# Performance work log

Measured on AMD Instinct MI355X. Metric: run time of the kernel, lower is better.

Reference implementation:

```python
import jax, jax.numpy as jnp
import numpy as np

TOP_K = 4

def setup_inputs() -> dict:
    key = jax.random.key(0)
    k1, k2, k3, k4 = jax.random.split(key, 4)
    B, S, D, E, H, O = 4, 2048, 1024, 8, 512, 1024
    x = jax.random.normal(k1, (B, S, D), dtype=jnp.float32)
    wg = jax.random.normal(k2, (E, D), dtype=jnp.float32) * 0.02
    w1 = jax.random.normal(k3, (E, H, D), dtype=jnp.float32) * 0.02
    w2 = jax.random.normal(k4, (E, O, H), dtype=jnp.float32) * 0.02
    return {"x": x, "wg": wg, "w1": w1, "w2": w2}

def reference(x, wg, w1, w2):
    # x: [B, S, D]; wg: [E, D]; w1: [E, H, D]; w2: [E, O, H]
    B, S, D = x.shape
    E = wg.shape[0]
    xt = x.reshape(B * S, D)                       # [N, D]
    logits = xt @ wg.T                              # [N, E] gate logits
    _, idx = jax.lax.top_k(logits, TOP_K)           # [N, k] selected experts
    N = xt.shape[0]
    # membership mask: 1.0 where expert e is among the token's top-k
    mask = jnp.zeros((N, E), dtype=x.dtype).at[jnp.arange(N)[:, None], idx].set(1.0)
    # dense per-expert FFN (relu MLP), then combine with unweighted sum over
    # the k selected experts (the original sums top-k outputs without gate weights)
    h = jax.nn.relu(jnp.einsum('nd,ehd->neh', xt, w1))   # [N, E, H]
    y = jnp.einsum('neh,eoh->neo', h, w2)                # [N, E, O]
    out = jnp.einsum('neo,ne->no', y, mask)              # [N, O]
    return out.reshape(B, S, -1)
```

## Files before the change

kernel.cpp:

```cpp
#include <hip/hip_runtime.h>

typedef float f32x4 __attribute__((ext_vector_type(4)));
typedef short bf16x8 __attribute__((ext_vector_type(8)));

#define NTOK 8192
#define DIM  1024
#define NE   8
#define NH   512
#define NO   1024

static __device__ __forceinline__ unsigned short f2bf(float f) {
  unsigned u = __float_as_uint(f);
  u += 0x7fffu + ((u >> 16) & 1u);
  return (unsigned short)(u >> 16);
}
static __device__ __forceinline__ unsigned pk2(float a, float b) {
  return (unsigned)f2bf(a) | ((unsigned)f2bf(b) << 16);
}

static __device__ __forceinline__ f32x4 mfma_bf16(bf16x8 a, bf16x8 b, f32x4 c) {
  return __builtin_amdgcn_mfma_f32_16x16x32_bf16(a, b, c, 0, 0, 0);
}

__global__ __launch_bounds__(256) void gate_kernel(
    const float* __restrict__ x, const float* __restrict__ wg,
    float* __restrict__ mask)
{
  const int lane = threadIdx.x & 63;
  const int wv = threadIdx.x >> 6;
  const int n = blockIdx.x * 4 + wv;
  const float* xr = x + (size_t)n * DIM;
  float4 v[4];
#pragma unroll
  for (int i = 0; i < 4; ++i) v[i] = *(const float4*)(xr + i * 256 + lane * 4);
  double logit[NE];
#pragma unroll
  for (int e = 0; e < NE; ++e) {
    const float* wr = wg + e * DIM;
    double s = 0.0;
#pragma unroll
    for (int i = 0; i < 4; ++i) {
      float4 g = *(const float4*)(wr + i * 256 + lane * 4);
      s += (double)v[i].x * g.x + (double)v[i].y * g.y +
           (double)v[i].z * g.z + (double)v[i].w * g.w;
    }
#pragma unroll
    for (int off = 32; off; off >>= 1) s += __shfl_down(s, off);
    logit[e] = s;
  }
  if (lane == 0) {
    unsigned sel = 0;
#pragma unroll
    for (int t = 0; t < 4; ++t) {
      int best = 0; double bv = -1.0e300;
#pragma unroll
      for (int e = 0; e < NE; ++e)
        if (!((sel >> e) & 1) && logit[e] > bv) { bv = logit[e]; best = e; }
      sel |= 1u << best;
    }
#pragma unroll
    for (int e = 0; e < NE; ++e)
      mask[(size_t)n * NE + e] = ((sel >> e) & 1) ? 1.0f : 0.0f;
  }
}

__global__ __launch_bounds__(256) void pack_w1_kernel(
    const float* __restrict__ w1, unsigned short* __restrict__ w1p)
{
  int t = blockIdx.x * 256 + threadIdx.x;
  int lane = t & 63, ks = (t >> 6) & 31, nt = (t >> 11) & 31, e = t >> 16;
  int r = nt * 16 + (lane & 15);
  int c = ks * 32 + (lane >> 4) * 8;
  const float* src = w1 + ((size_t)(e * 512 + r)) * 1024 + c;
  float4 f0 = *(const float4*)src;
  float4 f1 = *(const float4*)(src + 4);
  uint4 v;
  v.x = pk2(f0.x, f0.y); v.y = pk2(f0.z, f0.w);
  v.z = pk2(f1.x, f1.y); v.w = pk2(f1.z, f1.w);
  *(uint4*)(w1p + (size_t)t * 8) = v;
}

__global__ __launch_bounds__(256) void pack_w2_kernel(
    const float* __restrict__ w2, unsigned short* __restrict__ w2p)
{
  int t = blockIdx.x * 256 + threadIdx.x;
  int lane = t & 63, ks = (t >> 6) & 15, ot = (t >> 10) & 63, e = t >> 16;
  int o = ot * 16 + (lane & 15);
  int h = ks * 32 + (lane >> 4) * 8;
  const float* src = w2 + ((size_t)(e * 1024 + o)) * 512 + h;
  float4 f0 = *(const float4*)src;
  float4 f1 = *(const float4*)(src + 4);
  uint4 v;
  v.x = pk2(f0.x, f0.y); v.y = pk2(f0.z, f0.w);
  v.z = pk2(f1.x, f1.y); v.w = pk2(f1.z, f1.w);
  *(uint4*)(w2p + (size_t)t * 8) = v;
}

__global__ __launch_bounds__(1024, 4) void moe_ffn(
    const float* __restrict__ x, const unsigned short* __restrict__ w1p,
    const unsigned short* __restrict__ w2p, const float* __restrict__ mask,
    float* __restrict__ out)
{
  __shared__ unsigned short xs[64 * 64 * 8];
  __shared__ unsigned short hs[32 * 64 * 8];
  __shared__ float mk[32 * NE];

  const int tid = threadIdx.x;
  const int lane = tid & 63;
  const int wv = tid >> 6;
  const int row0 = blockIdx.x * 32;
  const int arow = lane & 15;
  const int kch = lane >> 4;

#pragma unroll
  for (int i = 0; i < 4; ++i) {
    int c = i * 1024 + tid;
    int r = c >> 7;
    int ch = c & 127;
    const float* src = x + (size_t)(row0 + r) * DIM + ch * 8;
    float4 f0 = *(const float4*)src;
    float4 f1 = *(const float4*)(src + 4);
    uint4 v;
    v.x = pk2(f0.x, f0.y); v.y = pk2(f0.z, f0.w);
    v.z = pk2(f1.x, f1.y); v.w = pk2(f1.z, f1.w);
    int f = (ch >> 2) * 2 + (r >> 4);
    int l = ((ch & 3) << 4) | (r & 15);
    *(uint4*)(xs + ((size_t)(f * 64 + l)) * 8) = v;
  }
  if (tid < 32 * NE) mk[tid] = mask[(size_t)row0 * NE + tid];
  __syncthreads();

  f32x4 oacc[2][4];
#pragma unroll
  for (int m = 0; m < 2; ++m)
#pragma unroll
    for (int n = 0; n < 4; ++n) oacc[m][n] = f32x4{0.f, 0.f, 0.f, 0.f};

  for (int e = 0; e < NE; ++e) {
    f32x4 hacc[2][2];
#pragma unroll
    for (int m = 0; m < 2; ++m)
#pragma unroll
      for (int n = 0; n < 2; ++n) hacc[m][n] = f32x4{0.f, 0.f, 0.f, 0.f};

    const unsigned short* b1 = w1p + ((size_t)(e * 32 + wv * 2) * 32) * 64 * 8;
#pragma unroll 4
    for (int ks = 0; ks < 32; ++ks) {
      bf16x8 a0 = *(const bf16x8*)(xs + ((size_t)((ks * 2 + 0) * 64 + lane)) * 8);
      bf16x8 a1 = *(const bf16x8*)(xs + ((size_t)((ks * 2 + 1) * 64 + lane)) * 8);
      bf16x8 b0 = *(const bf16x8*)(b1 + ((size_t)(0 * 32 + ks) * 64 + lane) * 8);
      bf16x8 b2 = *(const bf16x8*)(b1 + ((size_t)(1 * 32 + ks) * 64 + lane) * 8);
      hacc[0][0] = mfma_bf16(a0, b0, hacc[0][0]);
      hacc[1][0] = mfma_bf16(a1, b0, hacc[1][0]);
      hacc[0][1] = mfma_bf16(a0, b2, hacc[0][1]);
      hacc[1][1] = mfma_bf16(a1, b2, hacc[1][1]);
    }
    __syncthreads();

#pragma unroll
    for (int m = 0; m < 2; ++m)
#pragma unroll
      for (int n = 0; n < 2; ++n)
#pragma unroll
        for (int j = 0; j < 4; ++j) {
          float v = fmaxf(hacc[m][n][j], 0.0f) * mk[(m * 16 + kch * 4 + j) * NE + e];
          int l2 = ((n * 2 + (arow >> 3)) << 4) | (kch * 4 + j);
          hs[((size_t)((wv * 2 + m) * 64 + l2)) * 8 + (arow & 7)] = f2bf(v);
        }
    __syncthreads();

    const unsigned short* b2p = w2p + ((size_t)(e * 64 + wv * 4) * 16) * 64 * 8;
#pragma unroll 4
    for (int ks = 0; ks < 16; ++ks) {
      bf16x8 a0 = *(const bf16x8*)(hs + ((size_t)((ks * 2 + 0) * 64 + lane)) * 8);
      bf16x8 a1 = *(const bf16x8*)(hs + ((size_t)((ks * 2 + 1) * 64 + lane)) * 8);
#pragma unroll
      for (int n = 0; n < 4; ++n) {
        bf16x8 b = *(const bf16x8*)(b2p + ((size_t)(n * 16 + ks) * 64 + lane) * 8);
        oacc[0][n] = mfma_bf16(a0, b, oacc[0][n]);
        oacc[1][n] = mfma_bf16(a1, b, oacc[1][n]);
      }
    }
  }

#pragma unroll
  for (int m = 0; m < 2; ++m)
#pragma unroll
    for (int n = 0; n < 4; ++n)
#pragma unroll
      for (int j = 0; j < 4; ++j) {
        int row = row0 + m * 16 + kch * 4 + j;
        int col = wv * 64 + n * 16 + arow;
        out[(size_t)row * NO + col] = oacc[m][n][j];
      }
}

extern "C" void kernel_launch(void* const* d_in, const int* in_sizes, int n_in,
                              void* d_out, int out_size, void* d_ws, size_t ws_size,
                              hipStream_t stream) {
  (void)in_sizes; (void)n_in; (void)out_size; (void)ws_size;
  const float* x  = (const float*)d_in[0];
  const float* wg = (const float*)d_in[1];
  const float* w1 = (const float*)d_in[2];
  const float* w2 = (const float*)d_in[3];
  float* out = (float*)d_out;
  char* ws = (char*)d_ws;
  unsigned short* w1p = (unsigned short*)ws;
  unsigned short* w2p = (unsigned short*)(ws + ((size_t)8 << 20));
  float* mask = (float*)(ws + ((size_t)16 << 20));

  gate_kernel<<<2048, 256, 0, stream>>>(x, wg, mask);
  pack_w1_kernel<<<2048, 256, 0, stream>>>(w1, w1p);
  pack_w2_kernel<<<2048, 256, 0, stream>>>(w2, w2p);
  moe_ffn<<<256, 1024, 0, stream>>>(x, w1p, w2p, mask, out);
}
```

Before: 200.5 us.

## Retile MoE FFN to 64-row blocks split over output halves with bitmask gating

The FFN kernel now processes 64 tokens per block, with each block computing half of the output columns. Waves are arranged as a 4x4 grid over rows and columns, and the hidden dimension is processed in two halves per expert. The aim is more weight reuse per global load and more MFMAs per A fragment. The gate now writes a one-byte expert bitmask per token instead of eight floats, which cuts mask traffic and shared memory. In exchange, the first GEMM (x·W1) is recomputed by both column-half blocks, which doubles that work, and LDS use rises for the larger x tile.

```diff
diff --git a/kernel.cpp b/kernel.cpp
--- a/kernel.cpp
+++ b/kernel.cpp
@@ -24,7 +24,7 @@
 
 __global__ __launch_bounds__(256) void gate_kernel(
     const float* __restrict__ x, const float* __restrict__ wg,
-    float* __restrict__ mask)
+    unsigned char* __restrict__ msk8)
 {
   const int lane = threadIdx.x & 63;
   const int wv = threadIdx.x >> 6;
@@ -58,9 +58,7 @@
         if (!((sel >> e) & 1) && logit[e] > bv) { bv = logit[e]; best = e; }
       sel |= 1u << best;
     }
-#pragma unroll
-    for (int e = 0; e < NE; ++e)
-      mask[(size_t)n * NE + e] = ((sel >> e) & 1) ? 1.0f : 0.0f;
+    msk8[n] = (unsigned char)sel;
   }
 }
 
@@ -98,22 +96,24 @@
 
 __global__ __launch_bounds__(1024, 4) void moe_ffn(
     const float* __restrict__ x, const unsigned short* __restrict__ w1p,
-    const unsigned short* __restrict__ w2p, const float* __restrict__ mask,
+    const unsigned short* __restrict__ w2p, const unsigned char* __restrict__ msk8,
     float* __restrict__ out)
 {
-  __shared__ unsigned short xs[64 * 64 * 8];
+  __shared__ unsigned short xs[128 * 64 * 8];
   __shared__ unsigned short hs[32 * 64 * 8];
-  __shared__ float mk[32 * NE];
 
   const int tid = threadIdx.x;
   const int lane = tid & 63;
   const int wv = tid >> 6;
-  const int row0 = blockIdx.x * 32;
+  const int rw4 = wv & 3;
+  const int cw4 = wv >> 2;
+  const int row0 = (blockIdx.x >> 1) * 64;
+  const int z = blockIdx.x & 1;
   const int arow = lane & 15;
   const int kch = lane >> 4;
 
 #pragma unroll
-  for (int i = 0; i < 4; ++i) {
+  for (int i = 0; i < 8; ++i) {
     int c = i * 1024 + tid;
     int r = c >> 7;
     int ch = c & 127;
@@ -123,76 +123,74 @@
     uint4 v;
     v.x = pk2(f0.x, f0.y); v.y = pk2(f0.z, f0.w);
     v.z = pk2(f1.x, f1.y); v.w = pk2(f1.z, f1.w);
-    int f = (ch >> 2) * 2 + (r >> 4);
+    int f = (ch >> 2) * 4 + (r >> 4);
     int l = ((ch & 3) << 4) | (r & 15);
     *(uint4*)(xs + ((size_t)(f * 64 + l)) * 8) = v;
   }
-  if (tid < 32 * NE) mk[tid] = mask[(size_t)row0 * NE + tid];
+  const unsigned mbits = *(const unsigned*)(msk8 + row0 + rw4 * 16 + kch * 4);
   __syncthreads();
 
-  f32x4 oacc[2][4];
-#pragma unroll
-  for (int m = 0; m < 2; ++m)
-#pragma unroll
-    for (int n = 0; n < 4; ++n) oacc[m][n] = f32x4{0.f, 0.f, 0.f, 0.f};
+  const unsigned short* xp = xs + lane * 8;
+  const unsigned short* hp = hs + lane * 8;
+
+  f32x4 oacc[8];
+#pragma unroll
+  for (int n = 0; n < 8; ++n) oacc[n] = f32x4{0.f, 0.f, 0.f, 0.f};
 
   for (int e = 0; e < NE; ++e) {
-    f32x4 hacc[2][2];
-#pragma unroll
-    for (int m = 0; m < 2; ++m)
-#pragma unroll
-      for (int n = 0; n < 2; ++n) hacc[m][n] = f32x4{0.f, 0.f, 0.f, 0.f};
-
-    const unsigned short* b1 = w1p + ((size_t)(e * 32 + wv * 2) * 32) * 64 * 8;
-#pragma unroll 4
-    for (int ks = 0; ks < 32; ++ks) {
-      bf16x8 a0 = *(const bf16x8*)(xs + ((size_t)((ks * 2 + 0) * 64 + lane)) * 8);
-      bf16x8 a1 = *(const bf16x8*)(xs + ((size_t)((ks * 2 + 1) * 64 + lane)) * 8);
-      bf16x8 b0 = *(const bf16x8*)(b1 + ((size_t)(0 * 32 + ks) * 64 + lane) * 8);
-      bf16x8 b2 = *(const bf16x8*)(b1 + ((size_t)(1 * 32 + ks) * 64 + lane) * 8);
-      hacc[0][0] = mfma_bf16(a0, b0, hacc[0][0]);
-      hacc[1][0] = mfma_bf16(a1, b0, hacc[1][0]);
-      hacc[0][1] = mfma_bf16(a0, b2, hacc[0][1]);
-      hacc[1][1] = mfma_bf16(a1, b2, hacc[1][1]);
-    }
-    __syncthreads();
-
-#pragma unroll
-    for (int m = 0; m < 2; ++m)
-#pragma unroll
-      for (int n = 0; n < 2; ++n)
+#pragma unroll
+    for (int hh = 0; hh < 2; ++hh) {
+      f32x4 hacc[4];
+#pragma unroll
+      for (int n = 0; n < 4; ++n) hacc[n] = f32x4{0.f, 0.f, 0.f, 0.f};
+
+      const unsigned short* pb =
+          w1p + ((size_t)(e * 32 + hh * 16 + cw4 * 4) * 32) * 512 + lane * 8;
+#pragma unroll 2
+      for (int ks = 0; ks < 32; ++ks) {
+        bf16x8 a = *(const bf16x8*)(xp + (ks * 4 + rw4) * 512);
+#pragma unroll
+        for (int n = 0; n < 4; ++n) {
+          bf16x8 b = *(const bf16x8*)(pb + (size_t)n * 16384 + ks * 512);
+          hacc[n] = mfma_bf16(a, b, hacc[n]);
+        }
+      }
+      __syncthreads();
+
+#pragma unroll
+      for (int n = 0; n < 4; ++n)
 #pragma unroll
         for (int j = 0; j < 4; ++j) {
-          float v = fmaxf(hacc[m][n][j], 0.0f) * mk[(m * 16 + kch * 4 + j) * NE + e];
-          int l2 = ((n * 2 + (arow >> 3)) << 4) | (kch * 4 + j);
-          hs[((size_t)((wv * 2 + m) * 64 + l2)) * 8 + (arow & 7)] = f2bf(v);
+          float v = fmaxf(hacc[n][j], 0.0f);
+          v = ((mbits >> (j * 8 + e)) & 1u) ? v : 0.0f;
+          int f = (cw4 * 2 + (n >> 1)) * 4 + rw4;
+          int l2 = (((n & 1) * 2 + (arow >> 3)) << 4) | (kch * 4 + j);
+          hs[((size_t)(f * 64 + l2)) * 8 + (arow & 7)] = f2bf(v);
         }
-    __syncthreads();
-
-    const unsigned short* b2p = w2p + ((size_t)(e * 64 + wv * 4) * 16) * 64 * 8;
-#pragma unroll 4
-    for (int ks = 0; ks < 16; ++ks) {
-      bf16x8 a0 = *(const bf16x8*)(hs + ((size_t)((ks * 2 + 0) * 64 + lane)) * 8);
-      bf16x8 a1 = *(const bf16x8*)(hs + ((size_t)((ks * 2 + 1) * 64 + lane)) * 8);
-#pragma unroll
-      for (int n = 0; n < 4; ++n) {
-        bf16x8 b = *(const bf16x8*)(b2p + ((size_t)(n * 16 + ks) * 64 + lane) * 8);
-        oacc[0][n] = mfma_bf16(a0, b, oacc[0][n]);
-        oacc[1][n] = mfma_bf16(a1, b, oacc[1][n]);
+      __syncthreads();
+
+      const unsigned short* pc =
+          w2p + ((size_t)((e * 64 + z * 32 + cw4 * 8) * 16 + hh * 8)) * 512 + lane * 8;
+#pragma unroll 2
+      for (int ks2 = 0; ks2 < 8; ++ks2) {
+        bf16x8 a = *(const bf16x8*)(hp + (ks2 * 4 + rw4) * 512);
+#pragma unroll
+        for (int n = 0; n < 8; ++n) {
+          bf16x8 b = *(const bf16x8*)(pc + (size_t)n * 8192 + ks2 * 512);
+          oacc[n] = mfma_bf16(a, b, oacc[n]);
+        }
       }
     }
   }
 
 #pragma unroll
-  for (int m = 0; m < 2; ++m)
-#pragma unroll
-    for (int n = 0; n < 4; ++n)
-#pragma unroll
-      for (int j = 0; j < 4; ++j) {
-        int row = row0 + m * 16 + kch * 4 + j;
-        int col = wv * 64 + n * 16 + arow;
-        out[(size_t)row * NO + col] = oacc[m][n][j];
-      }
+  for (int n = 0; n < 8; ++n)
+#pragma unroll
+    for (int j = 0; j < 4; ++j) {
+      int row = row0 + rw4 * 16 + kch * 4 + j;
+      int col = z * 512 + (cw4 * 8 + n) * 16 + arow;
+      out[(size_t)row * NO + col] = oacc[n][j];
+    }
 }
 
 extern "C" void kernel_launch(void* const* d_in, const int* in_sizes, int n_in,
@@ -207,10 +205,10 @@
   char* ws = (char*)d_ws;
   unsigned short* w1p = (unsigned short*)ws;
   unsigned short* w2p = (unsigned short*)(ws + ((size_t)8 << 20));
-  float* mask = (float*)(ws + ((size_t)16 << 20));
-
-  gate_kernel<<<2048, 256, 0, stream>>>(x, wg, mask);
+  unsigned char* msk8 = (unsigned char*)(ws + ((size_t)16 << 20));
+
+  gate_kernel<<<2048, 256, 0, stream>>>(x, wg, msk8);
   pack_w1_kernel<<<2048, 256, 0, stream>>>(w1, w1p);
   pack_w2_kernel<<<2048, 256, 0, stream>>>(w2, w2p);
-  moe_ffn<<<256, 1024, 0, stream>>>(x, w1p, w2p, mask, out);
-}
+  moe_ffn<<<256, 1024, 0, stream>>>(x, w1p, w2p, msk8, out);
+}
```

Result: slower. 414.4 us (+106.6%).
